# Kernel tuning notes

Hardware: AMD Instinct MI355X
Metric: run time of the kernel (lower is better)

## Reference

```python
import jax, jax.numpy as jnp
import numpy as np


def _mlp(x, W0, b0, W1, b1, W2, b2, W3, b3):
    # nlayers=4 MLP: 3->128->128->128->3 with ReLU between layers
    h = jax.nn.relu(x @ W0 + b0)
    h = jax.nn.relu(h @ W1 + b1)
    h = jax.nn.relu(h @ W2 + b2)
    return h @ W3 + b3


def setup_inputs() -> dict:
    key = jax.random.key(0)
    ks = jax.random.split(key, 8)
    B, Nc, Nt, Dx, Dy, H = 8, 1024, 1024, 3, 32, 128
    s = lambda fan: 1.0 / np.sqrt(fan)
    return {
        "xc": jax.random.normal(ks[0], (B, Nc, Dx), jnp.float32),
        "yc": jax.random.normal(ks[1], (B, Nc, Dy), jnp.float32),
        "xt": jax.random.normal(ks[2], (B, Nt, Dx), jnp.float32),
        "W0": jax.random.normal(ks[3], (Dx, H), jnp.float32) * s(Dx),
        "b0": jnp.zeros((H,), jnp.float32),
        "W1": jax.random.normal(ks[4], (H, H), jnp.float32) * s(H),
        "b1": jnp.zeros((H,), jnp.float32),
        "W2": jax.random.normal(ks[5], (H, H), jnp.float32) * s(H),
        "b2": jnp.zeros((H,), jnp.float32),
        "W3": jax.random.normal(ks[6], (H, Dx), jnp.float32) * s(H),
        "b3": jnp.zeros((Dx,), jnp.float32),
    }


def reference(xc, yc, xt, W0, b0, W1, b1, W2, b2, W3, b3):
    # sigmas: per-target, per-coordinate positive scales  (B, Nt, Dx)
    sig = jnp.exp(_mlp(xt, W0, b0, W1, b1, W2, b2, W3, b3))
    # squared differences (B, Nc, Nt, Dx), scaled and reduced over Dx
    A = (xc[:, :, None, :] - xt[:, None, :, :]) ** 2
    P = -(A * sig[:, None, :, :]).sum(axis=3)        # (B, Nc, Nt)
    S = jax.nn.softmax(P, axis=1)                    # softmax over context
    # weighted average of context values: (B, Nt, Dy)
    return jnp.einsum("bnd,bnt->btd", yc, S)
```

## Files before the change

### kernel.cpp

```cpp
#include <hip/hip_runtime.h>
#include <math.h>

#define BB 8
#define NCC 1024
#define NTT 1024
#define HH 128
#define DYY 32
#define NTB 16
#define LOG2E 1.44269504088896340736f

#define HB 0
#define RED 2112
#define WCH 2496
#define YCB 0
#define XCB 4096
#define SIGL 7168
#define SMEM_SZ 7216
#define CMB 0
#define SL 4224
#define HSTRIDE 132


#define ACC16(E, PTR)                                                          \
    do {                                                                       \
        const float4* yv_ = (const float4*)(PTR);                              \
        const float4 q0_ = yv_[0], q1_ = yv_[1], q2_ = yv_[2], q3_ = yv_[3];   \
        acc[0] = fmaf(E, q0_.x, acc[0]);                                       \
        acc[1] = fmaf(E, q0_.y, acc[1]);                                       \
        acc[2] = fmaf(E, q0_.z, acc[2]);                                       \
        acc[3] = fmaf(E, q0_.w, acc[3]);                                       \
        acc[4] = fmaf(E, q1_.x, acc[4]);                                       \
        acc[5] = fmaf(E, q1_.y, acc[5]);                                       \
        acc[6] = fmaf(E, q1_.z, acc[6]);                                       \
        acc[7] = fmaf(E, q1_.w, acc[7]);                                       \
        acc[8] = fmaf(E, q2_.x, acc[8]);                                       \
        acc[9] = fmaf(E, q2_.y, acc[9]);                                       \
        acc[10] = fmaf(E, q2_.z, acc[10]);                                     \
        acc[11] = fmaf(E, q2_.w, acc[11]);                                     \
        acc[12] = fmaf(E, q3_.x, acc[12]);                                     \
        acc[13] = fmaf(E, q3_.y, acc[13]);                                     \
        acc[14] = fmaf(E, q3_.z, acc[14]);                                     \
        acc[15] = fmaf(E, q3_.w, acc[15]);                                     \
    } while (0)

__global__ __launch_bounds__(512, 2) void k_fused(const float* __restrict__ xc,
                                                  const float* __restrict__ yc,
                                                  const float* __restrict__ xt,
                                                  const float* __restrict__ W0,
                                                  const float* __restrict__ b0,
                                                  const float* __restrict__ W1,
                                                  const float* __restrict__ b1,
                                                  const float* __restrict__ W2,
                                                  const float* __restrict__ b2,
                                                  const float* __restrict__ W3,
                                                  const float* __restrict__ b3,
                                                  float* __restrict__ out) {
    const int tid = threadIdx.x;
    const int phys = blockIdx.x;
    const int bid = (phys & 7) * 64 + (phys >> 3);
    const int t0 = bid * NTB;
    const int b = bid >> 6;
    const int wv = tid >> 6;
    const int lane = tid & 63;

    __shared__ float smem[SMEM_SZ];

    const float4* __restrict__ ycG4 = (const float4*)(yc + (size_t)b * NCC * DYY);
    const float4* __restrict__ xcG4 = (const float4*)(xc + (size_t)b * NCC * 3);

    float* ycw = smem + YCB + wv * 512;
    float* xcw = smem + XCB + wv * 384;
    const int ybase = wv * 1024;

    const int jg = tid >> 4;
    const int p = tid & 15;
    const int j0 = jg * 4;
    const int jl4 = (jg & 3) * 4;
    float* hrow = smem + HB + p * HSTRIDE;

    {
        const float* xr = xt + (size_t)(t0 + p) * 3;
        const float x0 = xr[0], x1 = xr[1], x2 = xr[2];
        const float4* W0v = (const float4*)W0;
        const float4 w0a = W0v[jg], w0b = W0v[32 + jg], w0c = W0v[64 + jg];
        const float4 bb0 = ((const float4*)b0)[jg];
        float4 h0;
        h0.x = fmaxf(fmaf(x0, w0a.x, fmaf(x1, w0b.x, fmaf(x2, w0c.x, bb0.x))), 0.f);
        h0.y = fmaxf(fmaf(x0, w0a.y, fmaf(x1, w0b.y, fmaf(x2, w0c.y, bb0.y))), 0.f);
        h0.z = fmaxf(fmaf(x0, w0a.z, fmaf(x1, w0b.z, fmaf(x2, w0c.z, bb0.z))), 0.f);
        h0.w = fmaxf(fmaf(x0, w0a.w, fmaf(x1, w0b.w, fmaf(x2, w0c.w, bb0.w))), 0.f);
        *(float4*)(hrow + j0) = h0;
    }

    const int gWb = (lane >> 2) * 32 + wv * 4 + (lane & 3);
    float* wwb = smem + WCH + wv * 512;
    const float4* __restrict__ W1v = (const float4*)W1;
    const float4* __restrict__ W2v = (const float4*)W2;

    float4 wA0 = W1v[gWb], wA1 = W1v[gWb + 512];
    __syncthreads();

    auto run_layer = [&](const float4* __restrict__ Wv, const float4 bi,
                         float4 r0, float4 r1) -> float4 {
        float a0 = bi.x, a1 = bi.y, a2 = bi.z, a3 = bi.w;
        ((float4*)wwb)[lane] = r0;
        float4 wcur = r1;
#pragma unroll
        for (int c = 0; c < 8; ++c) {
            float4 wnext;
            if (c < 6) wnext = Wv[gWb + (c + 2) * 512];
            if (c < 7) ((float4*)(wwb + ((c + 1) & 1) * 256))[lane] = wcur;
            const float* wbc = wwb + (c & 1) * 256;
#pragma unroll
            for (int q = 0; q < 4; ++q) {
                const float4 ch = *(const float4*)(hrow + c * 16 + q * 4);
                const float4 k0 = *(const float4*)(wbc + (q * 4 + 0) * 16 + jl4);
                const float4 k1 = *(const float4*)(wbc + (q * 4 + 1) * 16 + jl4);
                const float4 k2 = *(const float4*)(wbc + (q * 4 + 2) * 16 + jl4);
                const float4 k3 = *(const float4*)(wbc + (q * 4 + 3) * 16 + jl4);
                a0 = fmaf(ch.x, k0.x, a0);
                a1 = fmaf(ch.x, k0.y, a1);
                a2 = fmaf(ch.x, k0.z, a2);
                a3 = fmaf(ch.x, k0.w, a3);
                a0 = fmaf(ch.y, k1.x, a0);
                a1 = fmaf(ch.y, k1.y, a1);
                a2 = fmaf(ch.y, k1.z, a2);
                a3 = fmaf(ch.y, k1.w, a3);
                a0 = fmaf(ch.z, k2.x, a0);
                a1 = fmaf(ch.z, k2.y, a1);
                a2 = fmaf(ch.z, k2.z, a2);
                a3 = fmaf(ch.z, k2.w, a3);
                a0 = fmaf(ch.w, k3.x, a0);
                a1 = fmaf(ch.w, k3.y, a1);
                a2 = fmaf(ch.w, k3.z, a2);
                a3 = fmaf(ch.w, k3.w, a3);
            }
            wcur = wnext;
        }
        float4 r;
        r.x = fmaxf(a0, 0.f);
        r.y = fmaxf(a1, 0.f);
        r.z = fmaxf(a2, 0.f);
        r.w = fmaxf(a3, 0.f);
        return r;
    };

    float4 oL1 = run_layer(W1v, ((const float4*)b1)[jg], wA0, wA1);
    float4 wB0 = W2v[gWb], wB1 = W2v[gWb + 512];
    __syncthreads();
    *(float4*)(hrow + j0) = oL1;
    __syncthreads();
    float4 oL2 = run_layer(W2v, ((const float4*)b2)[jg], wB0, wB1);

    {
        const float4* W3v = (const float4*)W3;
        const float4 wr0 = W3v[jg * 3 + 0];
        const float4 wr1 = W3v[jg * 3 + 1];
        const float4 wr2 = W3v[jg * 3 + 2];
        float p0 = oL2.x * wr0.x + oL2.y * wr0.w + oL2.z * wr1.z + oL2.w * wr2.y;
        float p1 = oL2.x * wr0.y + oL2.y * wr1.x + oL2.z * wr1.w + oL2.w * wr2.z;
        float p2 = oL2.x * wr0.z + oL2.y * wr1.y + oL2.z * wr2.x + oL2.w * wr2.w;
        p0 += __shfl_xor(p0, 16, 64);
        p0 += __shfl_xor(p0, 32, 64);
        p1 += __shfl_xor(p1, 16, 64);
        p1 += __shfl_xor(p1, 32, 64);
        p2 += __shfl_xor(p2, 16, 64);
        p2 += __shfl_xor(p2, 32, 64);
        if (lane < 16) {
            smem[RED + wv * 48 + lane * 3 + 0] = p0;
            smem[RED + wv * 48 + lane * 3 + 1] = p1;
            smem[RED + wv * 48 + lane * 3 + 2] = p2;
        }
    }
    __syncthreads();
    if (tid < 48) {
        const int r = tid / 3, cix = tid - r * 3;
        float v = b3[cix];
#pragma unroll
        for (int g = 0; g < 8; ++g) v += smem[RED + g * 48 + r * 3 + cix];
        smem[SIGL + r * 3 + cix] = __expf(v) * LOG2E;
    }
    __syncthreads();

    {
        float4 ty0 = ycG4[ybase + lane];
        float4 ty1 = ycG4[ybase + 64 + lane];
        ((float4*)ycw)[lane] = ty0;
        ((float4*)(ycw + 256))[lane] = ty1;
        if (lane < 48) {
            float4 tx0 = xcG4[wv * 96 + lane];
            float4 tx1 = xcG4[wv * 96 + 48 + lane];
            ((float4*)xcw)[lane] = tx0;
            ((float4*)xcw)[lane + 48] = tx1;
        }
    }

    const int tl = lane & 15;
    const int dg = (lane >> 4) & 1;
    const int ns = lane >> 5;
    const int dg16 = dg * 16;
    const int rown = ns * 4 + dg * 2;
    const int rowo = ns * 4 + 2 - dg * 2;

    const float s0 = smem[SIGL + tl * 3 + 0];
    const float s1 = smem[SIGL + tl * 3 + 1];
    const float s2 = smem[SIGL + tl * 3 + 2];
    const float* ar = xt + (size_t)(t0 + tl) * 3;
    const float a0 = ar[0], a1 = ar[1], a2 = ar[2];

    float acc[16];
#pragma unroll
    for (int i = 0; i < 16; ++i) acc[i] = 0.f;
    float l = 0.f;

#pragma unroll 2
    for (int t = 0; t < 16; ++t) {
        float4 ynext;
        if (t < 14) ynext = ycG4[ybase + (t + 2) * 64 + lane];
        const float* yb = ycw + (t & 1) * 256;
        const float* xb = xcw + t * 24;

        float d0 = xb[rown * 3 + 0] - a0;
        float d1 = xb[rown * 3 + 1] - a1;
        float d2 = xb[rown * 3 + 2] - a2;
        float pp = fmaf(s0, d0 * d0, fmaf(s1, d1 * d1, s2 * (d2 * d2)));
        const float eo0 = exp2f(-pp);
        d0 = xb[rown * 3 + 3] - a0;
        d1 = xb[rown * 3 + 4] - a1;
        d2 = xb[rown * 3 + 5] - a2;
        pp = fmaf(s0, d0 * d0, fmaf(s1, d1 * d1, s2 * (d2 * d2)));
        const float eo1 = exp2f(-pp);
        l += eo0 + eo1;
        const float ex0 = __shfl_xor(eo0, 16, 64);
        const float ex1 = __shfl_xor(eo1, 16, 64);

        ACC16(eo0, yb + rown * 32 + dg16);
        ACC16(eo1, yb + (rown + 1) * 32 + dg16);
        ACC16(ex0, yb + rowo * 32 + dg16);
        ACC16(ex1, yb + (rowo + 1) * 32 + dg16);

        if (t < 14)
            ((float4*)(ycw + (t & 1) * 256))[lane] = ynext;
    }

    l += __shfl_xor(l, 16, 64);
#pragma unroll
    for (int i = 0; i < 16; ++i) acc[i] += __shfl_xor(acc[i], 32, 64);
    l += __shfl_xor(l, 32, 64);

    __syncthreads();
    if (ns == 0) {
#pragma unroll
        for (int i = 0; i < 16; ++i)
            smem[CMB + (wv * 16 + tl) * 33 + dg16 + i] = acc[i];
        if (dg == 0) smem[SL + wv * 16 + tl] = l;
    }
    __syncthreads();
    {
        const int rtl = tid >> 5, d = tid & 31;
        float ssum = 0.f, lsum = 0.f;
#pragma unroll
        for (int ww = 0; ww < 8; ++ww) {
            ssum += smem[CMB + (ww * 16 + rtl) * 33 + d];
            lsum += smem[SL + ww * 16 + rtl];
        }
        out[(size_t)(t0 + rtl) * DYY + d] = ssum / lsum;
    }
}

extern "C" void kernel_launch(void* const* d_in, const int* in_sizes, int n_in,
                              void* d_out, int out_size, void* d_ws, size_t ws_size,
                              hipStream_t stream) {
    const float* xc = (const float*)d_in[0];
    const float* yc = (const float*)d_in[1];
    const float* xt = (const float*)d_in[2];
    const float* W0 = (const float*)d_in[3];
    const float* b0 = (const float*)d_in[4];
    const float* W1 = (const float*)d_in[5];
    const float* b1 = (const float*)d_in[6];
    const float* W2 = (const float*)d_in[7];
    const float* b2 = (const float*)d_in[8];
    const float* W3 = (const float*)d_in[9];
    const float* b3 = (const float*)d_in[10];
    float* out = (float*)d_out;

    k_fused<<<dim3(BB * NTT / NTB), dim3(512), 0, stream>>>(xc, yc, xt, W0, b0,
                                                            W1, b1, W2, b2, W3,
                                                            b3, out);
}
```

Before: 105.7 us.

## Compute softmax-weighted yc sum with fp16 MFMA instead of scalar FMAs

Replaces the scalar FMA accumulation of exp weights times yc with MFMA 16x16x32 f16 instructions. Exp weights are packed into fp16 A fragments, and yc is loaded column-wise, converted to fp16 and transposed into shared memory as the B operand, with the next chunk prefetched while the current one computes. This cuts VALU work in the inner loop. In exchange it loses precision (fp16 weights and values), adds strided global loads of yc, and changes the final cross-wave reduction layout.

```diff
diff --git a/kernel.cpp b/kernel.cpp
--- a/kernel.cpp
+++ b/kernel.cpp
@@ -9,39 +9,17 @@
 #define NTB 16
 #define LOG2E 1.44269504088896340736f
 
+typedef _Float16 half8 __attribute__((ext_vector_type(8)));
+typedef float f32x4 __attribute__((ext_vector_type(4)));
+
 #define HB 0
 #define RED 2112
 #define WCH 2496
-#define YCB 0
-#define XCB 4096
-#define SIGL 7168
-#define SMEM_SZ 7216
+#define SIGL 8192
+#define SMEM_SZ 8240
 #define CMB 0
 #define SL 4224
 #define HSTRIDE 132
-
-
-#define ACC16(E, PTR)                                                          \
-    do {                                                                       \
-        const float4* yv_ = (const float4*)(PTR);                              \
-        const float4 q0_ = yv_[0], q1_ = yv_[1], q2_ = yv_[2], q3_ = yv_[3];   \
-        acc[0] = fmaf(E, q0_.x, acc[0]);                                       \
-        acc[1] = fmaf(E, q0_.y, acc[1]);                                       \
-        acc[2] = fmaf(E, q0_.z, acc[2]);                                       \
-        acc[3] = fmaf(E, q0_.w, acc[3]);                                       \
-        acc[4] = fmaf(E, q1_.x, acc[4]);                                       \
-        acc[5] = fmaf(E, q1_.y, acc[5]);                                       \
-        acc[6] = fmaf(E, q1_.z, acc[6]);                                       \
-        acc[7] = fmaf(E, q1_.w, acc[7]);                                       \
-        acc[8] = fmaf(E, q2_.x, acc[8]);                                       \
-        acc[9] = fmaf(E, q2_.y, acc[9]);                                       \
-        acc[10] = fmaf(E, q2_.z, acc[10]);                                     \
-        acc[11] = fmaf(E, q2_.w, acc[11]);                                     \
-        acc[12] = fmaf(E, q3_.x, acc[12]);                                     \
-        acc[13] = fmaf(E, q3_.y, acc[13]);                                     \
-        acc[14] = fmaf(E, q3_.z, acc[14]);                                     \
-        acc[15] = fmaf(E, q3_.w, acc[15]);                                     \
-    } while (0)
 
 __global__ __launch_bounds__(512, 2) void k_fused(const float* __restrict__ xc,
                                                   const float* __restrict__ yc,
@@ -65,12 +43,7 @@
 
     __shared__ float smem[SMEM_SZ];
 
-    const float4* __restrict__ ycG4 = (const float4*)(yc + (size_t)b * NCC * DYY);
     const float4* __restrict__ xcG4 = (const float4*)(xc + (size_t)b * NCC * 3);
-
-    float* ycw = smem + YCB + wv * 512;
-    float* xcw = smem + XCB + wv * 384;
-    const int ybase = wv * 1024;
 
     const int jg = tid >> 4;
     const int p = tid & 15;
@@ -177,30 +150,15 @@
         const int r = tid / 3, cix = tid - r * 3;
         float v = b3[cix];
 #pragma unroll
-        for (int g = 0; g < 8; ++g) v += smem[RED + g * 48 + r * 3 + cix];
+        for (int g2 = 0; g2 < 8; ++g2) v += smem[RED + g2 * 48 + r * 3 + cix];
         smem[SIGL + r * 3 + cix] = __expf(v) * LOG2E;
     }
     __syncthreads();
 
-    {
-        float4 ty0 = ycG4[ybase + lane];
-        float4 ty1 = ycG4[ybase + 64 + lane];
-        ((float4*)ycw)[lane] = ty0;
-        ((float4*)(ycw + 256))[lane] = ty1;
-        if (lane < 48) {
-            float4 tx0 = xcG4[wv * 96 + lane];
-            float4 tx1 = xcG4[wv * 96 + 48 + lane];
-            ((float4*)xcw)[lane] = tx0;
-            ((float4*)xcw)[lane + 48] = tx1;
-        }
-    }
-
     const int tl = lane & 15;
-    const int dg = (lane >> 4) & 1;
-    const int ns = lane >> 5;
-    const int dg16 = dg * 16;
-    const int rown = ns * 4 + dg * 2;
-    const int rowo = ns * 4 + 2 - dg * 2;
+    const int g = lane >> 4;
+    const int sd = lane & 31;
+    const int snr = lane >> 5;
 
     const float s0 = smem[SIGL + tl * 3 + 0];
     const float s1 = smem[SIGL + tl * 3 + 1];
@@ -208,64 +166,91 @@
     const float* ar = xt + (size_t)(t0 + tl) * 3;
     const float a0 = ar[0], a1 = ar[1], a2 = ar[2];
 
-    float acc[16];
-#pragma unroll
-    for (int i = 0; i < 16; ++i) acc[i] = 0.f;
+    float* warena = smem + wv * 1024;
+    _Float16* ycT = (_Float16*)warena;
+    float* xcw = warena + 640;
+
+    if (lane < 48) {
+        float4 tx0 = xcG4[wv * 96 + lane];
+        float4 tx1 = xcG4[wv * 96 + 48 + lane];
+        ((float4*)xcw)[lane] = tx0;
+        ((float4*)xcw)[lane + 48] = tx1;
+    }
+
+    const float* ycol = yc + (size_t)b * NCC * DYY + (size_t)(wv * 128) * DYY + sd;
+    float ld[16];
+#define YLOAD(C)                                                               \
+    _Pragma("unroll") for (int q = 0; q < 16; ++q)                             \
+        ld[q] = ycol[(size_t)((C) * 32 + (q >> 3) * 16 + snr * 8 + (q & 7)) * DYY];
+#define YWRITE()                                                               \
+    do {                                                                       \
+        _Pragma("unroll") for (int r = 0; r < 2; ++r) {                        \
+            half8 pk;                                                          \
+            _Pragma("unroll") for (int j = 0; j < 8; ++j)                      \
+                pk[j] = (_Float16)ld[r * 8 + j];                               \
+            *(half8*)(ycT + sd * 40 + r * 16 + snr * 8) = pk;                  \
+        }                                                                      \
+    } while (0)
+
+    YLOAD(0);
+    YWRITE();
+
+    f32x4 acc0 = {0.f, 0.f, 0.f, 0.f};
+    f32x4 acc1 = {0.f, 0.f, 0.f, 0.f};
     float l = 0.f;
 
-#pragma unroll 2
-    for (int t = 0; t < 16; ++t) {
-        float4 ynext;
-        if (t < 14) ynext = ycG4[ybase + (t + 2) * 64 + lane];
-        const float* yb = ycw + (t & 1) * 256;
-        const float* xb = xcw + t * 24;
-
-        float d0 = xb[rown * 3 + 0] - a0;
-        float d1 = xb[rown * 3 + 1] - a1;
-        float d2 = xb[rown * 3 + 2] - a2;
-        float pp = fmaf(s0, d0 * d0, fmaf(s1, d1 * d1, s2 * (d2 * d2)));
-        const float eo0 = exp2f(-pp);
-        d0 = xb[rown * 3 + 3] - a0;
-        d1 = xb[rown * 3 + 4] - a1;
-        d2 = xb[rown * 3 + 5] - a2;
-        pp = fmaf(s0, d0 * d0, fmaf(s1, d1 * d1, s2 * (d2 * d2)));
-        const float eo1 = exp2f(-pp);
-        l += eo0 + eo1;
-        const float ex0 = __shfl_xor(eo0, 16, 64);
-        const float ex1 = __shfl_xor(eo1, 16, 64);
-
-        ACC16(eo0, yb + rown * 32 + dg16);
-        ACC16(eo1, yb + (rown + 1) * 32 + dg16);
-        ACC16(ex0, yb + rowo * 32 + dg16);
-        ACC16(ex1, yb + (rowo + 1) * 32 + dg16);
-
-        if (t < 14)
-            ((float4*)(ycw + (t & 1) * 256))[lane] = ynext;
+#pragma unroll
+    for (int c = 0; c < 4; ++c) {
+        if (c < 3) YLOAD(c + 1);
+
+        float xv[24];
+        {
+            const float4* xr4 = (const float4*)(xcw + (c * 32 + g * 8) * 3);
+#pragma unroll
+            for (int q = 0; q < 6; ++q) *(float4*)(xv + q * 4) = xr4[q];
+        }
+        half8 af;
+#pragma unroll
+        for (int i = 0; i < 8; ++i) {
+            const float d0 = xv[i * 3 + 0] - a0;
+            const float d1 = xv[i * 3 + 1] - a1;
+            const float d2 = xv[i * 3 + 2] - a2;
+            const float pp = fmaf(s0, d0 * d0, fmaf(s1, d1 * d1, s2 * (d2 * d2)));
+            const _Float16 eh = (_Float16)exp2f(-pp);
+            af[i] = eh;
+            l += (float)eh;
+        }
+        const half8 bf0 = *(const half8*)(ycT + tl * 40 + g * 8);
+        const half8 bf1 = *(const half8*)(ycT + (16 + tl) * 40 + g * 8);
+        acc0 = __builtin_amdgcn_mfma_f32_16x16x32_f16(af, bf0, acc0, 0, 0, 0);
+        acc1 = __builtin_amdgcn_mfma_f32_16x16x32_f16(af, bf1, acc1, 0, 0, 0);
+
+        if (c < 3) YWRITE();
     }
 
     l += __shfl_xor(l, 16, 64);
-#pragma unroll
-    for (int i = 0; i < 16; ++i) acc[i] += __shfl_xor(acc[i], 32, 64);
     l += __shfl_xor(l, 32, 64);
 
     __syncthreads();
-    if (ns == 0) {
-#pragma unroll
-        for (int i = 0; i < 16; ++i)
-            smem[CMB + (wv * 16 + tl) * 33 + dg16 + i] = acc[i];
-        if (dg == 0) smem[SL + wv * 16 + tl] = l;
-    }
+#pragma unroll
+    for (int r = 0; r < 4; ++r) {
+        smem[CMB + wv * 528 + (g * 4 + r) * 33 + tl] = acc0[r];
+        smem[CMB + wv * 528 + (g * 4 + r) * 33 + 16 + tl] = acc1[r];
+    }
+    if (lane < 16) smem[SL + wv * 16 + lane] = l;
     __syncthreads();
     {
-        const int rtl = tid >> 5, d = tid & 31;
-        float ssum = 0.f, lsum = 0.f;
-#pragma unroll
-        for (int ww = 0; ww < 8; ++ww) {
-            ssum += smem[CMB + (ww * 16 + rtl) * 33 + d];
-            lsum += smem[SL + ww * 16 + rtl];
-        }
-        out[(size_t)(t0 + rtl) * DYY + d] = ssum / lsum;
-    }
+        const int t = tid >> 5, d = tid & 31;
+        float s = 0.f, ls = 0.f;
+#pragma unroll
+        for (int w = 0; w < 8; ++w) {
+            s += smem[CMB + w * 528 + t * 33 + d];
+            ls += smem[SL + w * 16 + t];
+        }
+        out[(size_t)(t0 + t) * DYY + d] = s / ls;
+    }
+#undef YLOAD
+#undef YWRITE
 }
 
 extern "C" void kernel_launch(void* const* d_in, const int* in_sizes, int n_in,
```

Measured after the change: 91.90 us. 13.0% less time.
